# Optimization experiments

Hardware: AMD Instinct MI355X
Metric: run time of the kernel (lower is better)

The kernel has to match this reference:

```python
import jax, jax.numpy as jnp
import numpy as np

HEAD = 12
EPS = float(np.finfo(np.float32).eps)  # torch RMSNorm default eps = finfo(dtype).eps


def _rmsnorm(v, g):
    # v: [B,H,T,dh], g: [dh]
    ms = jnp.mean(v * v, axis=-1, keepdims=True)
    return v * jax.lax.rsqrt(ms + EPS) * g


def setup_inputs() -> dict:
    key = jax.random.key(0)
    k1, k2, k3, k4, k5 = jax.random.split(key, 5)
    B, T, C = 2, 2048, 768
    x = jax.random.normal(k1, (B, T, C), dtype=jnp.float32)
    # nn.Linear(feats, feats, bias=False) weight: [out, in]
    W = jax.random.normal(k2, (C, C), dtype=jnp.float32) * (1.0 / np.sqrt(C))
    dh = C // HEAD
    g1 = jnp.ones((dh,), dtype=jnp.float32)
    g2 = jnp.ones((dh,), dtype=jnp.float32)
    g3 = jnp.ones((dh,), dtype=jnp.float32)
    return {"x": x, "W": W, "g1": g1, "g2": g2, "g3": g3}


def reference(x, W, g1, g2, g3):
    B, T, C = x.shape
    dh = C // HEAD
    sqrt_d = np.sqrt(dh).astype(np.float32)
    # qkv projection (shared weights): w = x @ W.T -> [B,H,T,dh]
    w = (x @ W.T).reshape(B, T, HEAD, dh).transpose(0, 2, 1, 3)
    q = _rmsnorm(w, g1)
    k = _rmsnorm(w, g2)
    v = _rmsnorm(w, g3)
    # full T x T score matrix (intentionally materialized, as in the module)
    att = jnp.einsum('bhif,bhjf->bhij', q, k) / sqrt_d
    a = jax.nn.softmax(att, axis=-1) + jax.nn.softmax(att, axis=-2)  # bisoftmax
    y = jnp.einsum('bhij,bhjf->bihf', a, v).reshape(B, T, C)
    # F.linear(y, W.t()) == y @ W
    return y @ W
```

## Files before the change

kernel.cpp:

```cpp
#include <hip/hip_runtime.h>

constexpr int T_SEQ = 2048;
constexpr int CDIM  = 768;
constexpr int HEADS = 12;
constexpr int DH    = 64;
constexpr int BATCH = 2;
constexpr int BH_TOT = BATCH * HEADS;
constexpr int NROWS  = BATCH * T_SEQ;
constexpr float RMS_EPS = 1.1920929e-07f;
constexpr float QSCALE = 0.18033688011112042f;


typedef __attribute__((ext_vector_type(8))) short bf16x8;
typedef __attribute__((ext_vector_type(4))) float f32x4;
typedef __attribute__((ext_vector_type(4))) unsigned int u32x4;

__device__ __forceinline__ unsigned short f2bf(float f) {
    union { float f; unsigned int u; } v; v.f = f;
    unsigned int u = v.u;
    unsigned int r = (u + 0x7fffu + ((u >> 16) & 1u)) >> 16;
    return (unsigned short)r;
}
__device__ __forceinline__ float b2f(unsigned short h) {
    union { unsigned int u; float f; } v; v.u = ((unsigned int)h) << 16;
    return v.f;
}
__device__ __forceinline__ unsigned int cvt_pk_bf16(float lo, float hi) {
    unsigned int r;
    asm("v_cvt_pk_bf16_f32 %0, %1, %2" : "=v"(r) : "v"(lo), "v"(hi));
    return r;
}
__device__ __forceinline__ float fast_exp2(float x) {
    float r;
    asm("v_exp_f32 %0, %1" : "=v"(r) : "v"(x));
    return r;
}
__device__ __forceinline__ void gld_lds16(const void* g, void* l) {
    __builtin_amdgcn_global_load_lds(
        (const __attribute__((address_space(1))) void*)g,
        (__attribute__((address_space(3))) void*)l, 16, 0, 0);
}
__device__ __forceinline__ void stageLin(const unsigned short* g, unsigned short* l, int tid) {
#pragma unroll
    for (int p = 0; p < 4; ++p) {
        int d = (p * 256 + tid) * 16;
        gld_lds16((const char*)g + d, (char*)l + d);
    }
}
__device__ __forceinline__ void stage8k(const unsigned short* g, unsigned short* l, int tid) {
#pragma unroll
    for (int p = 0; p < 2; ++p) {
        int d = (p * 256 + tid) * 16;
        gld_lds16((const char*)g + d, (char*)l + d);
    }
}

__global__ __launch_bounds__(256) void prep_kernel(
    const float* __restrict__ x, const float* __restrict__ W,
    unsigned short* __restrict__ xh,
    unsigned short* __restrict__ Wh, unsigned short* __restrict__ WTh)
{
    const size_t NC = (size_t)NROWS * CDIM;
    const size_t WSZ = (size_t)CDIM * CDIM;
    size_t stride = (size_t)gridDim.x * blockDim.x;
    for (size_t i = (size_t)blockIdx.x * blockDim.x + threadIdx.x; i < NC; i += stride)
        xh[i] = f2bf(x[i]);
    for (size_t i = (size_t)blockIdx.x * blockDim.x + threadIdx.x; i < WSZ; i += stride) {
        unsigned short h = f2bf(W[i]);
        Wh[i] = h;
        size_t k = i / CDIM, c = i % CDIM;
        WTh[c * CDIM + k] = h;
    }
}

__global__ __launch_bounds__(256) void gemm64_nt(
    const unsigned short* __restrict__ A, const unsigned short* __restrict__ B,
    float* __restrict__ C, int M, int N, int K, int ldc)
{
    __shared__ unsigned short sA[2][64 * 64], sB[2][64 * 64];
    const int tid = threadIdx.x;
    const int lane = tid & 63;
    const int wv = tid >> 6;
    const int wr = wv >> 1, wc = wv & 1;
    const int li = lane & 15, g = lane >> 4;

    const int nbx = N / 64;
    const int wgid = blockIdx.x;
    const int xcd = wgid & 7;
    const int idx = wgid >> 3;
    const int perx = (M / 64) / 8;
    const int my = xcd * perx + idx / nbx;
    const int nx = idx % nbx;
    const int M0 = my * 64, N0 = nx * 64;

    f32x4 acc[2][2];
#pragma unroll
    for (int i = 0; i < 2; ++i)
#pragma unroll
        for (int j = 0; j < 2; ++j) acc[i][j] = (f32x4)0.0f;

#pragma unroll
    for (int p = 0; p < 2; ++p) {
        int dd = tid * 16 + p * 4096;
        int row = dd >> 7;
        int cb = (dd & 127) ^ ((row & 7) << 4);
        gld_lds16((const char*)A + ((size_t)(M0 + row) * K) * 2 + cb, (char*)sA[0] + dd);
        gld_lds16((const char*)B + ((size_t)(N0 + row) * K) * 2 + cb, (char*)sB[0] + dd);
    }

    int buf = 0;
    for (int k0 = 0; k0 < K; k0 += 64) {
        __syncthreads();
        if (k0 + 64 < K) {
#pragma unroll
            for (int p = 0; p < 2; ++p) {
                int dd = tid * 16 + p * 4096;
                int row = dd >> 7;
                int cb = (dd & 127) ^ ((row & 7) << 4);
                gld_lds16((const char*)A + ((size_t)(M0 + row) * K + k0 + 64) * 2 + cb,
                          (char*)sA[buf ^ 1] + dd);
                gld_lds16((const char*)B + ((size_t)(N0 + row) * K + k0 + 64) * 2 + cb,
                          (char*)sB[buf ^ 1] + dd);
            }
        }
#pragma unroll
        for (int ks = 0; ks < 2; ++ks) {
            const int ko = ks * 32 + g * 8;
            bf16x8 a[2], b[2];
#pragma unroll
            for (int mi = 0; mi < 2; ++mi) {
                int r = wr * 32 + mi * 16 + li;
                a[mi] = *(const bf16x8*)((char*)sA[buf] + ((r * 128 + ko * 2) ^ ((r & 7) << 4)));
            }
#pragma unroll
            for (int ni = 0; ni < 2; ++ni) {
                int r = wc * 32 + ni * 16 + li;
                b[ni] = *(const bf16x8*)((char*)sB[buf] + ((r * 128 + ko * 2) ^ ((r & 7) << 4)));
            }
#pragma unroll
            for (int mi = 0; mi < 2; ++mi)
#pragma unroll
                for (int ni = 0; ni < 2; ++ni)
                    acc[mi][ni] = __builtin_amdgcn_mfma_f32_16x16x32_bf16(a[mi], b[ni], acc[mi][ni], 0, 0, 0);
        }
        buf ^= 1;
    }
#pragma unroll
    for (int mi = 0; mi < 2; ++mi)
#pragma unroll
        for (int ni = 0; ni < 2; ++ni)
#pragma unroll
            for (int r = 0; r < 4; ++r) {
                int row = M0 + wr * 32 + mi * 16 + g * 4 + r;
                int col = N0 + wc * 32 + ni * 16 + li;
                C[(size_t)row * ldc + col] = acc[mi][ni][r];
            }
}

__global__ __launch_bounds__(256) void rmsqkv_kernel(
    const float* __restrict__ wbuf,
    const float* __restrict__ g1, const float* __restrict__ g2, const float* __restrict__ g3,
    unsigned short* __restrict__ qbf, unsigned short* __restrict__ kbf,
    unsigned short* __restrict__ vb)
{
    const int d = threadIdx.x & 63;
    const int wv = threadIdx.x >> 6;
    const int ridx = blockIdx.x * 4 + wv;
    const int bt = ridx / HEADS;
    const int h = ridx % HEADS;
    const int b = bt >> 11, t = bt & (T_SEQ - 1);

    float v = wbuf[(size_t)bt * CDIM + h * DH + d];
    float ss = v * v;
#pragma unroll
    for (int m = 32; m; m >>= 1) ss += __shfl_xor(ss, m);
    float r = rsqrtf(ss * (1.0f / 64.0f) + RMS_EPS);
    float wn = v * r;

    const int bh = b * HEADS + h;
    size_t fidx = (size_t)bh * (T_SEQ * DH)
                + (size_t)(t >> 7) * 8192
                + (size_t)((((t & 127) >> 4) * 2 + (d >> 5)) * 512
                           + ((d >> 3) & 3) * 128 + (t & 15) * 8 + (d & 7));
    qbf[fidx] = f2bf(wn * g1[d] * QSCALE);
    kbf[fidx] = f2bf(wn * g2[d]);
    vb[((size_t)bh * T_SEQ + t) * DH + d] = f2bf(wn * g3[d]);
}

__global__ __launch_bounds__(256) void vtrans_kernel(
    const unsigned short* __restrict__ vb, unsigned short* __restrict__ vTf)
{
    __shared__ unsigned short raw[128 * 72];
    const int bh = blockIdx.y, jt = blockIdx.x;
    const int tid = threadIdx.x;
    const unsigned short* src = &vb[((size_t)bh * T_SEQ + jt * 128) * DH];
#pragma unroll
    for (int p = 0; p < 4; ++p) {
        int i16 = p * 256 + tid;
        int r = i16 >> 3, c8 = i16 & 7;
        *(u32x4*)&raw[r * 72 + c8 * 8] = *(const u32x4*)&src[r * 64 + c8 * 8];
    }
    __syncthreads();
    unsigned short* dst = &vTf[(size_t)bh * (T_SEQ * DH) + (size_t)jt * 8192];
#pragma unroll
    for (int p = 0; p < 4; ++p) {
        int c = p * 256 + tid;
        int li = c & 15, g = (c >> 4) & 3, ni = (c >> 6) & 3, ks2 = c >> 8;
        int f = ni * 16 + li;
        int j0 = ks2 * 32 + g * 8;
        u32x4 out;
#pragma unroll
        for (int k = 0; k < 4; ++k) {
            unsigned int lo = raw[(j0 + 2 * k) * 72 + f];
            unsigned int hi = raw[(j0 + 2 * k + 1) * 72 + f];
            out[k] = lo | (hi << 16);
        }
        *(u32x4*)&dst[c * 8] = out;
    }
}

__global__ __launch_bounds__(256) void sums_kernel(
    const unsigned short* __restrict__ qbf, const unsigned short* __restrict__ kbf,
    float* __restrict__ rowsum, float* __restrict__ colsum)
{
    __shared__ unsigned short sQ[2][8192];
    const int tid = threadIdx.x;
    const int lane = tid & 63;
    const int w = tid >> 6;
    const int li = lane & 15;
    const int g = lane >> 4;

    const int wgid = blockIdx.x;
    const int xcd = wgid & 7;
    const int idx = wgid >> 3;
    const int bh = xcd * 3 + (idx >> 6);
    const int w2 = idx & 63;
    const int jx = w2 & 15;
    const int iy = w2 >> 4;
    const int J0 = jx * 128;

    const unsigned short* ktile = kbf + (size_t)bh * (T_SEQ * DH) + (size_t)jx * 8192;
    bf16x8 kf[2][2];
#pragma unroll
    for (int jb = 0; jb < 2; ++jb)
#pragma unroll
        for (int ks = 0; ks < 2; ++ks)
            kf[jb][ks] = *(const bf16x8*)&ktile[(size_t)((((w * 2 + jb) * 2 + ks) * 64 + lane) * 8)];

    const unsigned short* qbase = qbf + (size_t)bh * (T_SEQ * DH) + (size_t)(iy * 4) * 8192;
    stageLin(qbase, sQ[0], tid);
    __syncthreads();

    float csum[2][4];
#pragma unroll
    for (int jb = 0; jb < 2; ++jb)
#pragma unroll
        for (int r = 0; r < 4; ++r) csum[jb][r] = 0.0f;

    for (int it = 0; it < 4; ++it) {
        const int I0 = iy * 512 + it * 128;
        if (it + 1 < 4)
            stageLin(qbase + (size_t)(it + 1) * 8192, sQ[(it + 1) & 1], tid);
        const unsigned short* q = sQ[it & 1];

#pragma unroll
        for (int half = 0; half < 2; ++half) {
            f32x4 acc[2][4];
#pragma unroll
            for (int jb = 0; jb < 2; ++jb)
#pragma unroll
                for (int ib = 0; ib < 4; ++ib) acc[jb][ib] = (f32x4)0.0f;
#pragma unroll
            for (int ks = 0; ks < 2; ++ks) {
#pragma unroll
                for (int ib = 0; ib < 4; ++ib) {
                    bf16x8 qf = *(const bf16x8*)&q[(((half * 4 + ib) * 2 + ks) * 64 + lane) * 8];
#pragma unroll
                    for (int jb = 0; jb < 2; ++jb)
                        acc[jb][ib] = __builtin_amdgcn_mfma_f32_16x16x32_bf16(kf[jb][ks], qf, acc[jb][ib], 0, 0, 0);
                }
            }
#pragma unroll
            for (int ib = 0; ib < 4; ++ib) {
                float rp = 0.0f;
#pragma unroll
                for (int jb = 0; jb < 2; ++jb)
#pragma unroll
                    for (int r = 0; r < 4; ++r) {
                        float e = fast_exp2(acc[jb][ib][r]);
                        csum[jb][r] += e;
                        rp += e;
                    }
                rp += __shfl_xor(rp, 16);
                rp += __shfl_xor(rp, 32);
                if (g == 0)
                    atomicAdd(&rowsum[(size_t)bh * T_SEQ + I0 + half * 64 + ib * 16 + li], rp);
            }
        }
        __syncthreads();
    }
#pragma unroll
    for (int jb = 0; jb < 2; ++jb)
#pragma unroll
        for (int r = 0; r < 4; ++r) {
            float c = csum[jb][r];
            c += __shfl_xor(c, 1); c += __shfl_xor(c, 2);
            c += __shfl_xor(c, 4); c += __shfl_xor(c, 8);
            if (li == 0)
                atomicAdd(&colsum[(size_t)bh * T_SEQ + J0 + w * 32 + jb * 16 + g * 4 + r], c);
        }
}

__global__ __launch_bounds__(256) void inv_kernel(
    const float* __restrict__ rs, const float* __restrict__ cs,
    float* __restrict__ ri, float* __restrict__ ci_, int n)
{
    int i = blockIdx.x * 256 + threadIdx.x;
    if (i < n) { ri[i] = 1.0f / rs[i]; ci_[i] = 1.0f / cs[i]; }
}

__global__ __launch_bounds__(256) void fused_pv_kernel(
    const unsigned short* __restrict__ qbf, const unsigned short* __restrict__ kbf,
    const unsigned short* __restrict__ vTf,
    const float* __restrict__ rowinv, const float* __restrict__ colinv,
    unsigned short* __restrict__ yh)
{
    __shared__ unsigned short sK[4096];
    __shared__ unsigned short sV[4096];
    __shared__ unsigned short sP[4096];

    const int tid = threadIdx.x;
    const int lane = tid & 63;
    const int w = tid >> 6;
    const int li = lane & 15;
    const int g = lane >> 4;

    const int wgid = blockIdx.x;
    const int xcd = wgid & 7;
    const int idx = wgid >> 3;
    const int bh = xcd * 3 + (idx >> 5);
    const int it = idx & 31;
    const int I0 = it * 64;
    constexpr int NT = T_SEQ / 64;

    const int rbq = ((I0 & 127) >> 4) + w;
    const unsigned short* qtile = qbf + (size_t)bh * (T_SEQ * DH) + (size_t)(I0 >> 7) * 8192;
    bf16x8 qf[2];
#pragma unroll
    for (int ks = 0; ks < 2; ++ks)
        qf[ks] = *(const bf16x8*)&qtile[(size_t)(((rbq * 2 + ks) * 64 + lane) * 8)];
    const float rv = rowinv[bh * T_SEQ + I0 + w * 16 + li];

    char* const sPw = (char*)sP + w * 2048;

    f32x4 accy[4];
#pragma unroll
    for (int i = 0; i < 4; ++i) accy[i] = (f32x4)0.0f;

    const size_t bhbase = (size_t)bh * (T_SEQ * DH);
    const unsigned short* kt0 = kbf + bhbase;
    const unsigned short* vt0 = vTf + bhbase;

    stage8k(kt0, sK, tid);
    stage8k(vt0, sV, tid);
    __syncthreads();

    for (int jt = 0; jt < NT; ++jt) {
        f32x4 accs[4];
#pragma unroll
        for (int jb = 0; jb < 4; ++jb) accs[jb] = (f32x4)0.0f;
#pragma unroll
        for (int ks = 0; ks < 2; ++ks) {
#pragma unroll
            for (int jb = 0; jb < 4; ++jb) {
                bf16x8 kfr = *(const bf16x8*)&sK[((jb * 2 + ks) * 64 + lane) * 8];
                accs[jb] = __builtin_amdgcn_mfma_f32_16x16x32_bf16(kfr, qf[ks], accs[jb], 0, 0, 0);
            }
        }

#pragma unroll
        for (int jb = 0; jb < 4; ++jb) {
            f32x4 cv = *(const f32x4*)&colinv[(size_t)bh * T_SEQ + jt * 64 + jb * 16 + g * 4];
            float p0 = fast_exp2(accs[jb][0]) * (rv + cv[0]);
            float p1 = fast_exp2(accs[jb][1]) * (rv + cv[1]);
            float p2 = fast_exp2(accs[jb][2]) * (rv + cv[2]);
            float p3 = fast_exp2(accs[jb][3]) * (rv + cv[3]);
            uint2 pw;
            pw.x = cvt_pk_bf16(p0, p1);
            pw.y = cvt_pk_bf16(p2, p3);
            int off = ((jb >> 1) * 4 + (jb & 1) * 2 + (g >> 1)) * 256 + li * 16 + (g & 1) * 8;
            *(uint2*)(sPw + off) = pw;
        }

        __syncthreads();
        if (jt + 1 < NT)
            stage8k(kt0 + (size_t)(jt + 1) * 4096, sK, tid);

#pragma unroll
        for (int ks2 = 0; ks2 < 2; ++ks2) {
            bf16x8 pf = *(const bf16x8*)(sPw + ((ks2 * 4 + g) * 256 + li * 16));
#pragma unroll
            for (int ni = 0; ni < 4; ++ni) {
                bf16x8 vf = *(const bf16x8*)&sV[(ks2 * 256 + ni * 64 + lane) * 8];
                accy[ni] = __builtin_amdgcn_mfma_f32_16x16x32_bf16(pf, vf, accy[ni], 0, 0, 0);
            }
        }

        __syncthreads();
        if (jt + 1 < NT)
            stage8k(vt0 + (size_t)(jt + 1) * 4096, sV, tid);
    }

    const int b_ = bh / HEADS, h = bh % HEADS;
#pragma unroll
    for (int ni = 0; ni < 4; ++ni)
#pragma unroll
        for (int r = 0; r < 4; ++r) {
            int i = I0 + w * 16 + g * 4 + r;
            int col = h * DH + ni * 16 + li;
            yh[((size_t)b_ * T_SEQ + i) * CDIM + col] = f2bf(accy[ni][r]);
        }
}

extern "C" void kernel_launch(void* const* d_in, const int* in_sizes, int n_in,
                              void* d_out, int out_size, void* d_ws, size_t ws_size,
                              hipStream_t stream)
{
    const float* x  = (const float*)d_in[0];
    const float* W  = (const float*)d_in[1];
    const float* g1 = (const float*)d_in[2];
    const float* g2 = (const float*)d_in[3];
    const float* g3 = (const float*)d_in[4];
    float* out = (float*)d_out;

    char* p = (char*)d_ws;
    auto alloc = [&](size_t bytes) -> void* {
        void* r = (void*)p;
        p += (bytes + 255) & ~(size_t)255;
        return r;
    };
    const size_t NC  = (size_t)NROWS * CDIM;
    const size_t WSZ = (size_t)CDIM * CDIM;
    const size_t QSZ = (size_t)BH_TOT * T_SEQ * DH;

    unsigned short* xh   = (unsigned short*)alloc(NC * 2);
    unsigned short* Wh   = (unsigned short*)alloc(WSZ * 2);
    unsigned short* WTh  = (unsigned short*)alloc(WSZ * 2);
    float*          wbuf = (float*)alloc(NC * 4);
    unsigned short* qbf  = (unsigned short*)alloc(QSZ * 2);
    unsigned short* kbf  = (unsigned short*)alloc(QSZ * 2);
    unsigned short* vb   = (unsigned short*)alloc(QSZ * 2);
    unsigned short* vTf  = (unsigned short*)alloc(QSZ * 2);
    unsigned short* yh   = (unsigned short*)alloc(NC * 2);
    float* rowsum = (float*)alloc((size_t)BH_TOT * T_SEQ * 4);
    float* colsum = (float*)alloc((size_t)BH_TOT * T_SEQ * 4);
    float* rowinv = (float*)alloc((size_t)BH_TOT * T_SEQ * 4);
    float* colinv = (float*)alloc((size_t)BH_TOT * T_SEQ * 4);

    prep_kernel<<<2048, 256, 0, stream>>>(x, W, xh, Wh, WTh);
    gemm64_nt<<<(NROWS / 64) * (CDIM / 64), 256, 0, stream>>>(
        xh, Wh, wbuf, NROWS, CDIM, CDIM, CDIM);
    rmsqkv_kernel<<<(NROWS * HEADS) / 4, 256, 0, stream>>>(
        wbuf, g1, g2, g3, qbf, kbf, vb);
    vtrans_kernel<<<dim3(T_SEQ / 128, BH_TOT), 256, 0, stream>>>(vb, vTf);

    hipMemsetAsync(rowsum, 0, (size_t)BH_TOT * T_SEQ * 4, stream);
    hipMemsetAsync(colsum, 0, (size_t)BH_TOT * T_SEQ * 4, stream);
    sums_kernel<<<(T_SEQ / 128) * 4 * BH_TOT, 256, 0, stream>>>(
        qbf, kbf, rowsum, colsum);
    int n = BH_TOT * T_SEQ;
    inv_kernel<<<(n + 255) / 256, 256, 0, stream>>>(rowsum, colsum, rowinv, colinv, n);

    fused_pv_kernel<<<(T_SEQ / 64) * BH_TOT, 256, 0, stream>>>(
        qbf, kbf, vTf, rowinv, colinv, yh);

    gemm64_nt<<<(NROWS / 64) * (CDIM / 64), 256, 0, stream>>>(
        yh, WTh, out, NROWS, CDIM, CDIM, CDIM);
}
```

Baseline: 133.0 us.

## Double-buffer K/V tiles in fused PV kernel and fold reciprocal into it

Double-buffers K and V tiles in LDS so the next tile loads while the current one is computed, cutting per-iteration barriers from two to one. Removes the separate inv_kernel launch by taking reciprocals of row and column sums inline with the hardware rcp instruction. Merges the two memsets into one. In exchange it uses more LDS and adds a reciprocal per score element inside the loop, and the approximate rcp may lose a little precision.

Result: slower. 138.3 us (+4.0%).

```diff
diff --git a/kernel.cpp b/kernel.cpp
--- a/kernel.cpp
+++ b/kernel.cpp
@@ -34,6 +34,9 @@
     float r;
     asm("v_exp_f32 %0, %1" : "=v"(r) : "v"(x));
     return r;
+}
+__device__ __forceinline__ float fast_rcp(float x) {
+    return __builtin_amdgcn_rcpf(x);
 }
 __device__ __forceinline__ void gld_lds16(const void* g, void* l) {
     __builtin_amdgcn_global_load_lds(
@@ -311,22 +314,14 @@
         }
 }
 
-__global__ __launch_bounds__(256) void inv_kernel(
-    const float* __restrict__ rs, const float* __restrict__ cs,
-    float* __restrict__ ri, float* __restrict__ ci_, int n)
-{
-    int i = blockIdx.x * 256 + threadIdx.x;
-    if (i < n) { ri[i] = 1.0f / rs[i]; ci_[i] = 1.0f / cs[i]; }
-}
-
 __global__ __launch_bounds__(256) void fused_pv_kernel(
     const unsigned short* __restrict__ qbf, const unsigned short* __restrict__ kbf,
     const unsigned short* __restrict__ vTf,
-    const float* __restrict__ rowinv, const float* __restrict__ colinv,
+    const float* __restrict__ rowsum, const float* __restrict__ colsum,
     unsigned short* __restrict__ yh)
 {
-    __shared__ unsigned short sK[4096];
-    __shared__ unsigned short sV[4096];
+    __shared__ unsigned short sK[2][4096];
+    __shared__ unsigned short sV[2][4096];
     __shared__ unsigned short sP[4096];
 
     const int tid = threadIdx.x;
@@ -349,7 +344,7 @@
 #pragma unroll
     for (int ks = 0; ks < 2; ++ks)
         qf[ks] = *(const bf16x8*)&qtile[(size_t)(((rbq * 2 + ks) * 64 + lane) * 8)];
-    const float rv = rowinv[bh * T_SEQ + I0 + w * 16 + li];
+    const float rv = fast_rcp(rowsum[bh * T_SEQ + I0 + w * 16 + li]);
 
     char* const sPw = (char*)sP + w * 2048;
 
@@ -361,11 +356,17 @@
     const unsigned short* kt0 = kbf + bhbase;
     const unsigned short* vt0 = vTf + bhbase;
 
-    stage8k(kt0, sK, tid);
-    stage8k(vt0, sV, tid);
-    __syncthreads();
-
+    stage8k(kt0, sK[0], tid);
+    stage8k(vt0, sV[0], tid);
+
+    int buf = 0;
     for (int jt = 0; jt < NT; ++jt) {
+        __syncthreads();
+        if (jt + 1 < NT) {
+            stage8k(kt0 + (size_t)(jt + 1) * 4096, sK[buf ^ 1], tid);
+            stage8k(vt0 + (size_t)(jt + 1) * 4096, sV[buf ^ 1], tid);
+        }
+
         f32x4 accs[4];
 #pragma unroll
         for (int jb = 0; jb < 4; ++jb) accs[jb] = (f32x4)0.0f;
@@ -373,18 +374,18 @@
         for (int ks = 0; ks < 2; ++ks) {
 #pragma unroll
             for (int jb = 0; jb < 4; ++jb) {
-                bf16x8 kfr = *(const bf16x8*)&sK[((jb * 2 + ks) * 64 + lane) * 8];
+                bf16x8 kfr = *(const bf16x8*)&sK[buf][((jb * 2 + ks) * 64 + lane) * 8];
                 accs[jb] = __builtin_amdgcn_mfma_f32_16x16x32_bf16(kfr, qf[ks], accs[jb], 0, 0, 0);
             }
         }
 
 #pragma unroll
         for (int jb = 0; jb < 4; ++jb) {
-            f32x4 cv = *(const f32x4*)&colinv[(size_t)bh * T_SEQ + jt * 64 + jb * 16 + g * 4];
-            float p0 = fast_exp2(accs[jb][0]) * (rv + cv[0]);
-            float p1 = fast_exp2(accs[jb][1]) * (rv + cv[1]);
-            float p2 = fast_exp2(accs[jb][2]) * (rv + cv[2]);
-            float p3 = fast_exp2(accs[jb][3]) * (rv + cv[3]);
+            f32x4 cs = *(const f32x4*)&colsum[(size_t)bh * T_SEQ + jt * 64 + jb * 16 + g * 4];
+            float p0 = fast_exp2(accs[jb][0]) * (rv + fast_rcp(cs[0]));
+            float p1 = fast_exp2(accs[jb][1]) * (rv + fast_rcp(cs[1]));
+            float p2 = fast_exp2(accs[jb][2]) * (rv + fast_rcp(cs[2]));
+            float p3 = fast_exp2(accs[jb][3]) * (rv + fast_rcp(cs[3]));
             uint2 pw;
             pw.x = cvt_pk_bf16(p0, p1);
             pw.y = cvt_pk_bf16(p2, p3);
@@ -392,23 +393,16 @@
             *(uint2*)(sPw + off) = pw;
         }
 
-        __syncthreads();
-        if (jt + 1 < NT)
-            stage8k(kt0 + (size_t)(jt + 1) * 4096, sK, tid);
-
 #pragma unroll
         for (int ks2 = 0; ks2 < 2; ++ks2) {
             bf16x8 pf = *(const bf16x8*)(sPw + ((ks2 * 4 + g) * 256 + li * 16));
 #pragma unroll
             for (int ni = 0; ni < 4; ++ni) {
-                bf16x8 vf = *(const bf16x8*)&sV[(ks2 * 256 + ni * 64 + lane) * 8];
+                bf16x8 vf = *(const bf16x8*)&sV[buf][(ks2 * 256 + ni * 64 + lane) * 8];
                 accy[ni] = __builtin_amdgcn_mfma_f32_16x16x32_bf16(pf, vf, accy[ni], 0, 0, 0);
             }
         }
-
-        __syncthreads();
-        if (jt + 1 < NT)
-            stage8k(vt0 + (size_t)(jt + 1) * 4096, sV, tid);
+        buf ^= 1;
     }
 
     const int b_ = bh / HEADS, h = bh % HEADS;
@@ -452,10 +446,8 @@
     unsigned short* vb   = (unsigned short*)alloc(QSZ * 2);
     unsigned short* vTf  = (unsigned short*)alloc(QSZ * 2);
     unsigned short* yh   = (unsigned short*)alloc(NC * 2);
-    float* rowsum = (float*)alloc((size_t)BH_TOT * T_SEQ * 4);
-    float* colsum = (float*)alloc((size_t)BH_TOT * T_SEQ * 4);
-    float* rowinv = (float*)alloc((size_t)BH_TOT * T_SEQ * 4);
-    float* colinv = (float*)alloc((size_t)BH_TOT * T_SEQ * 4);
+    float* rowsum = (float*)alloc((size_t)BH_TOT * T_SEQ * 4 * 2);
+    float* colsum = rowsum + (size_t)BH_TOT * T_SEQ;
 
     prep_kernel<<<2048, 256, 0, stream>>>(x, W, xh, Wh, WTh);
     gemm64_nt<<<(NROWS / 64) * (CDIM / 64), 256, 0, stream>>>(
@@ -464,15 +456,12 @@
         wbuf, g1, g2, g3, qbf, kbf, vb);
     vtrans_kernel<<<dim3(T_SEQ / 128, BH_TOT), 256, 0, stream>>>(vb, vTf);
 
-    hipMemsetAsync(rowsum, 0, (size_t)BH_TOT * T_SEQ * 4, stream);
-    hipMemsetAsync(colsum, 0, (size_t)BH_TOT * T_SEQ * 4, stream);
+    hipMemsetAsync(rowsum, 0, (size_t)BH_TOT * T_SEQ * 4 * 2, stream);
     sums_kernel<<<(T_SEQ / 128) * 4 * BH_TOT, 256, 0, stream>>>(
         qbf, kbf, rowsum, colsum);
-    int n = BH_TOT * T_SEQ;
-    inv_kernel<<<(n + 255) / 256, 256, 0, stream>>>(rowsum, colsum, rowinv, colinv, n);
 
     fused_pv_kernel<<<(T_SEQ / 64) * BH_TOT, 256, 0, stream>>>(
-        qbf, kbf, vTf, rowinv, colinv, yh);
+        qbf, kbf, vTf, rowsum, colsum, yh);
 
     gemm64_nt<<<(NROWS / 64) * (CDIM / 64), 256, 0, stream>>>(
         yh, WTh, out, NROWS, CDIM, CDIM, CDIM);
```
